# Kernel optimization log

Measured on AMD Instinct MI355X. Metric: run time of the kernel, lower is better.

## Reference

```python
import jax, jax.numpy as jnp
import numpy as np

D = 512      # model dim
H = 8        # heads
HD = D // H  # head dim = 64
NQ = 2048    # n_query
NC = 4096    # n_context
EPS = 1e-5   # LayerNorm eps (torch default)


def setup_inputs() -> dict:
    key = jax.random.key(0)
    ks = jax.random.split(key, 12)
    s = 0.02
    return {
        "query_repr": jax.random.normal(ks[0], (NQ, D), dtype=jnp.float32),
        "context_repr": jax.random.normal(ks[1], (NC, D), dtype=jnp.float32),
        "query_coords": jax.random.uniform(ks[2], (NQ, 2), dtype=jnp.float32) * 10.0,
        "context_coords": jax.random.uniform(ks[3], (NC, 2), dtype=jnp.float32) * 10.0,
        "Wq": jax.random.normal(ks[4], (D, D), dtype=jnp.float32) * s,
        "bq": jnp.zeros((D,), jnp.float32),
        "Wk": jax.random.normal(ks[5], (D, D), dtype=jnp.float32) * s,
        "bk": jnp.zeros((D,), jnp.float32),
        "Wv": jax.random.normal(ks[6], (D, D), dtype=jnp.float32) * s,
        "bv": jnp.zeros((D,), jnp.float32),
        "Wo": jax.random.normal(ks[7], (D, D), dtype=jnp.float32) * s,
        "bo": jnp.zeros((D,), jnp.float32),
        "ln_g": jnp.ones((D,), jnp.float32),
        "ln_b": jnp.zeros((D,), jnp.float32),
        "log_scale": jnp.array(0.0, jnp.float32),          # log_distance_scale
        "bias_per_head": jnp.ones((H,), jnp.float32),      # distance_bias_per_head
    }


def reference(query_repr, context_repr, query_coords, context_coords,
              Wq, bq, Wk, bk, Wv, bv, Wo, bo, ln_g, ln_b,
              log_scale, bias_per_head):
    # pairwise Euclidean distances (NQ, NC)
    diff = query_coords[:, None, :] - context_coords[None, :, :]
    dist = jnp.sqrt(jnp.sum(diff * diff, axis=-1))
    # per-head additive attention bias (H, NQ, NC)
    bias = (-jnp.exp(log_scale) * dist)[None, :, :] * bias_per_head[:, None, None]

    # multi-head attention (batch=1, eval mode so dropout is identity)
    q = (query_repr @ Wq.T + bq).reshape(NQ, H, HD).transpose(1, 0, 2)    # (H, NQ, HD)
    k = (context_repr @ Wk.T + bk).reshape(NC, H, HD).transpose(1, 0, 2)  # (H, NC, HD)
    v = (context_repr @ Wv.T + bv).reshape(NC, H, HD).transpose(1, 0, 2)  # (H, NC, HD)

    scale = 1.0 / jnp.sqrt(jnp.float32(HD))
    scores = jnp.einsum('hqd,hkd->hqk', q, k) * scale + bias              # (H, NQ, NC)
    attn = jax.nn.softmax(scores, axis=-1)
    ctx = jnp.einsum('hqk,hkd->hqd', attn, v)                             # (H, NQ, HD)
    attended = ctx.transpose(1, 0, 2).reshape(NQ, D) @ Wo.T + bo          # (NQ, D)

    # residual + LayerNorm
    x = attended + query_repr
    mu = jnp.mean(x, axis=-1, keepdims=True)
    var = jnp.mean((x - mu) ** 2, axis=-1, keepdims=True)
    return (x - mu) / jnp.sqrt(var + EPS) * ln_g + ln_b
```

## Files before the change

### kernel.cpp

```cpp
#include <hip/hip_runtime.h>

#define D 512
#define H 8
#define HD 64
#define NQ 2048
#define NC 4096
#define SPLIT 8
#define CLEN (NC / SPLIT)
#define NT (CLEN / 32)
#define M0 3.0f
#define KP2 136
#define VP 40

#define TBM 128
#define TBN 64
#define TBK 32
#define TPAD 40

typedef __attribute__((ext_vector_type(8))) short short8;
typedef __attribute__((ext_vector_type(4))) short short4v;
typedef __attribute__((ext_vector_type(4))) float float4v;
typedef __attribute__((ext_vector_type(4))) int int4v;

__device__ inline float bf2f(short s) {
    unsigned int u = ((unsigned int)(unsigned short)s) << 16;
    return __builtin_bit_cast(float, u);
}
__device__ inline short f2bf(float f) {
    unsigned int u = __builtin_bit_cast(unsigned int, f);
    u = (u + 0x7FFF + ((u >> 16) & 1)) >> 16;
    return (short)u;
}
__device__ inline int cvtpk(float a, float b) {
    int w;
    asm("v_cvt_pk_bf16_f32 %0, %1, %2" : "=v"(w) : "v"(a), "v"(b));
    return w;
}

__global__ __launch_bounds__(256) void cast_all(
    const float* __restrict__ s0, const float* __restrict__ s1,
    const float* __restrict__ s2, const float* __restrict__ s3,
    const float* __restrict__ s4, const float* __restrict__ s5,
    short* __restrict__ dst)
{
    int i = blockIdx.x * 256 + threadIdx.x;
    const float* src; int off;
    if      (i < 262144) { src = s0; off = i; }
    else if (i < 786432) { src = s1; off = i - 262144; }
    else if (i < 851968) { src = s2; off = i - 786432; }
    else if (i < 917504) { src = s3; off = i - 851968; }
    else if (i < 983040) { src = s4; off = i - 917504; }
    else                 { src = s5; off = i - 983040; }
    float4v v = ((const float4v*)src)[off];
    short4v o;
    o.x = f2bf(v.x); o.y = f2bf(v.y); o.z = f2bf(v.z); o.w = f2bf(v.w);
    ((short4v*)dst)[i] = o;
}

__global__ __launch_bounds__(256) void gemm_bt_bias(
    const short* __restrict__ X, const short* __restrict__ W,
    const float* __restrict__ bias, short* __restrict__ out, int M)
{
    int wave = threadIdx.x >> 6, lane = threadIdx.x & 63;
    int gt = blockIdx.x * 4 + wave;
    int tm = gt >> 3;
    int tg = gt & 7;
    if (tm >= (M >> 4)) return;
    int l15 = lane & 15, quad = lane >> 4;
    const short* xp = X + (tm * 16 + l15) * D + quad * 8;
    const short* wp = W + (tg * 64 + l15) * D + quad * 8;
    float4v a0 = {0,0,0,0}, a1 = {0,0,0,0}, a2 = {0,0,0,0}, a3 = {0,0,0,0};
#pragma unroll
    for (int k = 0; k < D; k += 32) {
        short8 a  = *(const short8*)(xp + k);
        short8 b0 = *(const short8*)(wp + k);
        short8 b1 = *(const short8*)(wp + 16 * D + k);
        short8 b2 = *(const short8*)(wp + 32 * D + k);
        short8 b3 = *(const short8*)(wp + 48 * D + k);
        a0 = __builtin_amdgcn_mfma_f32_16x16x32_bf16(a, b0, a0, 0, 0, 0);
        a1 = __builtin_amdgcn_mfma_f32_16x16x32_bf16(a, b1, a1, 0, 0, 0);
        a2 = __builtin_amdgcn_mfma_f32_16x16x32_bf16(a, b2, a2, 0, 0, 0);
        a3 = __builtin_amdgcn_mfma_f32_16x16x32_bf16(a, b3, a3, 0, 0, 0);
    }
    int orow = tm * 16 + quad * 4;
    float4v accs[4] = {a0, a1, a2, a3};
#pragma unroll
    for (int j = 0; j < 4; j++) {
        int col = tg * 64 + j * 16 + l15;
        float bv = bias[col];
#pragma unroll
        for (int r = 0; r < 4; r++)
            out[(orow + r) * D + col] = f2bf(accs[j][r] + bv);
    }
}

__global__ __launch_bounds__(256) void gemm_qkv_tiled(
    const short* __restrict__ Xq, const short* __restrict__ Xc,
    const short* __restrict__ Wq, const short* __restrict__ Wk,
    const short* __restrict__ Wv,
    const float* __restrict__ bq, const float* __restrict__ bk,
    const float* __restrict__ bv,
    short* __restrict__ Qout, short* __restrict__ Kout,
    short* __restrict__ VoutT)
{
    __shared__ __align__(16) short Ab[2][TBM * TPAD];
    __shared__ __align__(16) short Bb[2][TBN * TPAD];

    int tid = threadIdx.x;
    int wave = tid >> 6, lane = tid & 63;
    int quad = lane >> 4, l15 = lane & 15;

    int blk = blockIdx.x;
    const short *X, *W;
    const float* bias;
    short* outp;
    int bm, bn, vmode;
    if (blk < 128) {
        X = Xq; W = Wq; bias = bq; outp = Qout; vmode = 0;
        bm = (blk >> 3) * TBM; bn = (blk & 7) * TBN;
    } else if (blk < 384) {
        int b = blk - 128;
        X = Xc; W = Wk; bias = bk; outp = Kout; vmode = 0;
        bm = (b >> 3) * TBM; bn = (b & 7) * TBN;
    } else {
        int b = blk - 384;
        X = Xc; W = Wv; bias = bv; outp = VoutT; vmode = 1;
        bm = (b >> 3) * TBM; bn = (b & 7) * TBN;
    }

    int ar = tid >> 1, ac = (tid & 1) * 16;
    int br = tid >> 2, bc = (tid & 3) * 8;
    const short* ag = X + (size_t)(bm + ar) * D + ac;
    const short* bg = W + (size_t)(bn + br) * D + bc;
    short* aw0 = &Ab[0][ar * TPAD + ac];
    short* aw1 = &Ab[1][ar * TPAD + ac];
    short* bw0 = &Bb[0][br * TPAD + bc];
    short* bw1 = &Bb[1][br * TPAD + bc];

    short8 ra0, ra1, rb;

#define GLOAD(ks) { const short* ap_ = ag + (ks) * TBK;                        \
        ra0 = *(const short8*)(ap_);                                           \
        ra1 = *(const short8*)(ap_ + 8);                                       \
        rb  = *(const short8*)(bg + (ks) * TBK); }
#define GDSW0 { *(short8*)aw0 = ra0; *(short8*)(aw0 + 8) = ra1;                \
                *(short8*)bw0 = rb; }
#define GDSW1 { *(short8*)aw1 = ra0; *(short8*)(aw1 + 8) = ra1;                \
                *(short8*)bw1 = rb; }

    float4v c00 = {0,0,0,0}, c01 = {0,0,0,0}, c02 = {0,0,0,0}, c03 = {0,0,0,0};
    float4v c10 = {0,0,0,0}, c11 = {0,0,0,0}, c12 = {0,0,0,0}, c13 = {0,0,0,0};

#define GCOMP(B)                                                               \
    {                                                                          \
        const short* abase = &Ab[B][(wave * 32 + l15) * TPAD + quad * 8];      \
        const short* bbase = &Bb[B][l15 * TPAD + quad * 8];                    \
        short8 a0 = *(const short8*)(abase);                                   \
        short8 a1 = *(const short8*)(abase + 16 * TPAD);                       \
        short8 b0 = *(const short8*)(bbase);                                   \
        short8 b1 = *(const short8*)(bbase + 16 * TPAD);                       \
        short8 b2 = *(const short8*)(bbase + 32 * TPAD);                       \
        short8 b3 = *(const short8*)(bbase + 48 * TPAD);                       \
        c00 = __builtin_amdgcn_mfma_f32_16x16x32_bf16(a0, b0, c00, 0, 0, 0);   \
        c01 = __builtin_amdgcn_mfma_f32_16x16x32_bf16(a0, b1, c01, 0, 0, 0);   \
        c02 = __builtin_amdgcn_mfma_f32_16x16x32_bf16(a0, b2, c02, 0, 0, 0);   \
        c03 = __builtin_amdgcn_mfma_f32_16x16x32_bf16(a0, b3, c03, 0, 0, 0);   \
        c10 = __builtin_amdgcn_mfma_f32_16x16x32_bf16(a1, b0, c10, 0, 0, 0);   \
        c11 = __builtin_amdgcn_mfma_f32_16x16x32_bf16(a1, b1, c11, 0, 0, 0);   \
        c12 = __builtin_amdgcn_mfma_f32_16x16x32_bf16(a1, b2, c12, 0, 0, 0);   \
        c13 = __builtin_amdgcn_mfma_f32_16x16x32_bf16(a1, b3, c13, 0, 0, 0);   \
    }

    GLOAD(0);
    GDSW0;
    GLOAD(1);
    __syncthreads();

    for (int t = 0; t < 14; t += 2) {
        GDSW1;
        GLOAD(t + 2);
        GCOMP(0);
        __syncthreads();
        GDSW0;
        GLOAD(t + 3);
        GCOMP(1);
        __syncthreads();
    }
    GDSW1;
    GCOMP(0);
    __syncthreads();
    GCOMP(1);

#undef GLOAD
#undef GDSW0
#undef GDSW1
#undef GCOMP

    float4v accs[2][4] = {{c00, c01, c02, c03}, {c10, c11, c12, c13}};
    if (vmode == 0) {
#pragma unroll
        for (int mf = 0; mf < 2; mf++) {
            int orow = bm + wave * 32 + mf * 16 + quad * 4;
#pragma unroll
            for (int nf = 0; nf < 4; nf++) {
                int col = bn + nf * 16 + l15;
                float bb_ = bias[col];
#pragma unroll
                for (int r = 0; r < 4; r++)
                    outp[(size_t)(orow + r) * D + col] = f2bf(accs[mf][nf][r] + bb_);
            }
        }
    } else {
#pragma unroll
        for (int mf = 0; mf < 2; mf++) {
            int orow = bm + wave * 32 + mf * 16 + quad * 4;
            int a = (orow & 31) >> 2;
            int posb = (a < 4) ? (8 * a) : (8 * (a - 4) + 4);
            int cp = (orow & ~31) + posb;
#pragma unroll
            for (int nf = 0; nf < 4; nf++) {
                int col = bn + nf * 16 + l15;
                float bb_ = bias[col];
                short4v o;
#pragma unroll
                for (int r = 0; r < 4; r++) o[r] = f2bf(accs[mf][nf][r] + bb_);
                *(short4v*)(outp + (size_t)col * NC + cp) = o;
            }
        }
    }
}

__global__ __launch_bounds__(256) void gemm_out_tiled(
    const short* __restrict__ X, const short* __restrict__ W,
    const float* __restrict__ bias, const float* __restrict__ resid,
    float* __restrict__ out)
{
    __shared__ __align__(16) short Ab[2][TBM * TPAD];
    __shared__ __align__(16) short Bb[2][TBN * TPAD];

    int tid = threadIdx.x;
    int wave = tid >> 6, lane = tid & 63;
    int quad = lane >> 4, l15 = lane & 15;

    int blk = blockIdx.x;
    int bm = (blk >> 3) * TBM, bn = (blk & 7) * TBN;

    int ar = tid >> 1, ac = (tid & 1) * 16;
    int br = tid >> 2, bc = (tid & 3) * 8;
    const short* ag = X + (size_t)(bm + ar) * D + ac;
    const short* bg = W + (size_t)(bn + br) * D + bc;
    short* aw0 = &Ab[0][ar * TPAD + ac];
    short* aw1 = &Ab[1][ar * TPAD + ac];
    short* bw0 = &Bb[0][br * TPAD + bc];
    short* bw1 = &Bb[1][br * TPAD + bc];

    short8 ra0, ra1, rb;

#define GLOAD(ks) { const short* ap_ = ag + (ks) * TBK;                        \
        ra0 = *(const short8*)(ap_);                                           \
        ra1 = *(const short8*)(ap_ + 8);                                       \
        rb  = *(const short8*)(bg + (ks) * TBK); }
#define GDSW0 { *(short8*)aw0 = ra0; *(short8*)(aw0 + 8) = ra1;                \
                *(short8*)bw0 = rb; }
#define GDSW1 { *(short8*)aw1 = ra0; *(short8*)(aw1 + 8) = ra1;                \
                *(short8*)bw1 = rb; }

    float4v c00 = {0,0,0,0}, c01 = {0,0,0,0}, c02 = {0,0,0,0}, c03 = {0,0,0,0};
    float4v c10 = {0,0,0,0}, c11 = {0,0,0,0}, c12 = {0,0,0,0}, c13 = {0,0,0,0};

#define GCOMP(B)                                                               \
    {                                                                          \
        const short* abase = &Ab[B][(wave * 32 + l15) * TPAD + quad * 8];      \
        const short* bbase = &Bb[B][l15 * TPAD + quad * 8];                    \
        short8 a0 = *(const short8*)(abase);                                   \
        short8 a1 = *(const short8*)(abase + 16 * TPAD);                       \
        short8 b0 = *(const short8*)(bbase);                                   \
        short8 b1 = *(const short8*)(bbase + 16 * TPAD);                       \
        short8 b2 = *(const short8*)(bbase + 32 * TPAD);                       \
        short8 b3 = *(const short8*)(bbase + 48 * TPAD);                       \
        c00 = __builtin_amdgcn_mfma_f32_16x16x32_bf16(a0, b0, c00, 0, 0, 0);   \
        c01 = __builtin_amdgcn_mfma_f32_16x16x32_bf16(a0, b1, c01, 0, 0, 0);   \
        c02 = __builtin_amdgcn_mfma_f32_16x16x32_bf16(a0, b2, c02, 0, 0, 0);   \
        c03 = __builtin_amdgcn_mfma_f32_16x16x32_bf16(a0, b3, c03, 0, 0, 0);   \
        c10 = __builtin_amdgcn_mfma_f32_16x16x32_bf16(a1, b0, c10, 0, 0, 0);   \
        c11 = __builtin_amdgcn_mfma_f32_16x16x32_bf16(a1, b1, c11, 0, 0, 0);   \
        c12 = __builtin_amdgcn_mfma_f32_16x16x32_bf16(a1, b2, c12, 0, 0, 0);   \
        c13 = __builtin_amdgcn_mfma_f32_16x16x32_bf16(a1, b3, c13, 0, 0, 0);   \
    }

    GLOAD(0);
    GDSW0;
    GLOAD(1);
    __syncthreads();

    for (int t = 0; t < 14; t += 2) {
        GDSW1;
        GLOAD(t + 2);
        GCOMP(0);
        __syncthreads();
        GDSW0;
        GLOAD(t + 3);
        GCOMP(1);
        __syncthreads();
    }
    GDSW1;
    GCOMP(0);
    __syncthreads();
    GCOMP(1);

#undef GLOAD
#undef GDSW0
#undef GDSW1
#undef GCOMP

    float4v accs[2][4] = {{c00, c01, c02, c03}, {c10, c11, c12, c13}};
#pragma unroll
    for (int mf = 0; mf < 2; mf++) {
        int orow = bm + wave * 32 + mf * 16 + quad * 4;
#pragma unroll
        for (int nf = 0; nf < 4; nf++) {
            int col = bn + nf * 16 + l15;
            float bb_ = bias[col];
#pragma unroll
            for (int r = 0; r < 4; r++)
                out[(size_t)(orow + r) * D + col] =
                    accs[mf][nf][r] + bb_ + resid[(size_t)(orow + r) * D + col];
        }
    }
}

__global__ __launch_bounds__(256) void gemm_bt_bias_res_f32(
    const short* __restrict__ X, const short* __restrict__ W,
    const float* __restrict__ bias, const float* __restrict__ resid,
    float* __restrict__ out, int M)
{
    int wave = threadIdx.x >> 6, lane = threadIdx.x & 63;
    int gt = blockIdx.x * 4 + wave;
    int tm = gt >> 3;
    int tg = gt & 7;
    if (tm >= (M >> 4)) return;
    int l15 = lane & 15, quad = lane >> 4;
    const short* xp = X + (tm * 16 + l15) * D + quad * 8;
    const short* wp = W + (tg * 64 + l15) * D + quad * 8;
    float4v a0 = {0,0,0,0}, a1 = {0,0,0,0}, a2 = {0,0,0,0}, a3 = {0,0,0,0};
#pragma unroll
    for (int k = 0; k < D; k += 32) {
        short8 a  = *(const short8*)(xp + k);
        short8 b0 = *(const short8*)(wp + k);
        short8 b1 = *(const short8*)(wp + 16 * D + k);
        short8 b2 = *(const short8*)(wp + 32 * D + k);
        short8 b3 = *(const short8*)(wp + 48 * D + k);
        a0 = __builtin_amdgcn_mfma_f32_16x16x32_bf16(a, b0, a0, 0, 0, 0);
        a1 = __builtin_amdgcn_mfma_f32_16x16x32_bf16(a, b1, a1, 0, 0, 0);
        a2 = __builtin_amdgcn_mfma_f32_16x16x32_bf16(a, b2, a2, 0, 0, 0);
        a3 = __builtin_amdgcn_mfma_f32_16x16x32_bf16(a, b3, a3, 0, 0, 0);
    }
    int orow = tm * 16 + quad * 4;
    float4v accs[4] = {a0, a1, a2, a3};
#pragma unroll
    for (int j = 0; j < 4; j++) {
        int col = tg * 64 + j * 16 + l15;
        float bv = bias[col];
#pragma unroll
        for (int r = 0; r < 4; r++) {
            int q = orow + r;
            out[q * D + col] = accs[j][r] + bv + resid[q * D + col];
        }
    }
}

__global__ __launch_bounds__(256) void attn_mfma_split9(
    const short* __restrict__ Q, const short* __restrict__ K,
    const short* __restrict__ Vp,
    const float* __restrict__ qc, const float* __restrict__ cc,
    const float* __restrict__ log_scale, const float* __restrict__ bph,
    short* __restrict__ Opart, float* __restrict__ Lpart)
{
    __shared__ __align__(16) short Klds[2][32 * KP2];
    __shared__ __align__(16) short Vlds[2][128 * VP];
    __shared__ __align__(16) float ccl[512];

    int tid = threadIdx.x;
    int wave = tid >> 6, lane = tid & 63;
    int h0 = blockIdx.y * 2;
    int sp = blockIdx.z;
    int q0 = blockIdx.x * 64 + wave * 16;
    int quad = lane >> 4, l15 = lane & 15;
    int cbase = sp * CLEN;

    const float LOG2E = 1.4426950408889634f;
    const float escale = 0.125f * LOG2E;
    const float M0L = M0 * LOG2E;
    float ebase = __expf(log_scale[0]);
    float bh0 = ebase * bph[h0] * LOG2E;
    float bh1 = ebase * bph[h0 + 1] * LOG2E;

    const short* qp = Q + (q0 + l15) * D + h0 * HD + quad * 8;
    short8 qa0_0 = *(const short8*)(qp);
    short8 qa1_0 = *(const short8*)(qp + 32);
    short8 qa0_1 = *(const short8*)(qp + 64);
    short8 qa1_1 = *(const short8*)(qp + 96);

    float qx = qc[(q0 + l15) * 2];
    float qy = qc[(q0 + l15) * 2 + 1];

    float lacc0 = 0.f, lacc1 = 0.f;
    float4v O00 = {0,0,0,0}, O01 = {0,0,0,0}, O02 = {0,0,0,0}, O03 = {0,0,0,0};
    float4v O10 = {0,0,0,0}, O11 = {0,0,0,0}, O12 = {0,0,0,0}, O13 = {0,0,0,0};

    int kr_ = tid >> 3, kc_ = tid & 7;
    int vr_ = tid >> 2, vc_ = tid & 3;
    const short* kg  = K + (size_t)h0 * HD + kc_ * 8;
    const short* vg0 = Vp + (size_t)(h0 * HD + vr_) * NC + vc_ * 8;
    const short* vg1 = Vp + (size_t)(h0 * HD + 64 + vr_) * NC + vc_ * 8;
    short* kw0a = &Klds[0][kr_ * KP2 + kc_ * 8];
    short* kw1a = &Klds[1][kr_ * KP2 + kc_ * 8];
    short* vw0a = &Vlds[0][vr_ * VP + vc_ * 8];
    short* vw0b = &Vlds[0][(64 + vr_) * VP + vc_ * 8];
    short* vw1a = &Vlds[1][vr_ * VP + vc_ * 8];
    short* vw1b = &Vlds[1][(64 + vr_) * VP + vc_ * 8];

    short8 rka, rkb, rva, rvb;

#define LOADR(c0_)                                                             \
    {                                                                          \
        const short* kp_ = kg + (size_t)((c0_) + kr_) * D;                     \
        rka = *(const short8*)(kp_);                                           \
        rkb = *(const short8*)(kp_ + 64);                                      \
        rva = *(const short8*)(vg0 + (c0_));                                   \
        rvb = *(const short8*)(vg1 + (c0_));                                   \
    }

#define DSW0 { *(short8*)kw0a = rka; *(short8*)(kw0a + 64) = rkb;              \
               *(short8*)vw0a = rva; *(short8*)vw0b = rvb; }
#define DSW1 { *(short8*)kw1a = rka; *(short8*)(kw1a + 64) = rkb;              \
               *(short8*)vw1a = rva; *(short8*)vw1b = rvb; }

    const float2* ccp = (const float2*)ccl;

#define HEAD(hoff, QA0, QA1, BH, LACC, OA, OB, OC, OD)                         \
    {                                                                          \
        short8 k00 = *(const short8*)(kb + l15 * KP2 + (hoff) + quad * 8);     \
        short8 k01 = *(const short8*)(kb + l15 * KP2 + (hoff) + 32 + quad * 8);\
        short8 k10 = *(const short8*)(kb + (16 + l15) * KP2 + (hoff) + quad * 8);\
        short8 k11 = *(const short8*)(kb + (16 + l15) * KP2 + (hoff) + 32 + quad * 8);\
        float4v s0 = {0,0,0,0}, s1 = {0,0,0,0};                                \
        s0 = __builtin_amdgcn_mfma_f32_16x16x32_bf16(k00, QA0, s0, 0, 0, 0);   \
        s0 = __builtin_amdgcn_mfma_f32_16x16x32_bf16(k01, QA1, s0, 0, 0, 0);   \
        s1 = __builtin_amdgcn_mfma_f32_16x16x32_bf16(k10, QA0, s1, 0, 0, 0);   \
        s1 = __builtin_amdgcn_mfma_f32_16x16x32_bf16(k11, QA1, s1, 0, 0, 0);   \
        short8 v0 = *(const short8*)(vb + ((hoff) / 64 * 64 + l15) * VP + quad * 8);       \
        short8 v1 = *(const short8*)(vb + ((hoff) / 64 * 64 + 16 + l15) * VP + quad * 8);  \
        short8 v2 = *(const short8*)(vb + ((hoff) / 64 * 64 + 32 + l15) * VP + quad * 8);  \
        short8 v3 = *(const short8*)(vb + ((hoff) / 64 * 64 + 48 + l15) * VP + quad * 8);  \
        float p00 = exp2f(__fmaf_rn(s0[0], escale, __fmaf_rn(-(BH), dA0, -M0L)));\
        float p01 = exp2f(__fmaf_rn(s0[1], escale, __fmaf_rn(-(BH), dA1, -M0L)));\
        float p02 = exp2f(__fmaf_rn(s0[2], escale, __fmaf_rn(-(BH), dA2, -M0L)));\
        float p03 = exp2f(__fmaf_rn(s0[3], escale, __fmaf_rn(-(BH), dA3, -M0L)));\
        float p10 = exp2f(__fmaf_rn(s1[0], escale, __fmaf_rn(-(BH), dB0, -M0L)));\
        float p11 = exp2f(__fmaf_rn(s1[1], escale, __fmaf_rn(-(BH), dB1, -M0L)));\
        float p12 = exp2f(__fmaf_rn(s1[2], escale, __fmaf_rn(-(BH), dB2, -M0L)));\
        float p13 = exp2f(__fmaf_rn(s1[3], escale, __fmaf_rn(-(BH), dB3, -M0L)));\
        LACC += ((p00 + p01) + (p02 + p03)) + ((p10 + p11) + (p12 + p13));     \
        int4v pw;                                                              \
        pw.x = cvtpk(p00, p01); pw.y = cvtpk(p02, p03);                        \
        pw.z = cvtpk(p10, p11); pw.w = cvtpk(p12, p13);                        \
        short8 pa = __builtin_bit_cast(short8, pw);                            \
        OA = __builtin_amdgcn_mfma_f32_16x16x32_bf16(pa, v0, OA, 0, 0, 0);     \
        OB = __builtin_amdgcn_mfma_f32_16x16x32_bf16(pa, v1, OB, 0, 0, 0);     \
        OC = __builtin_amdgcn_mfma_f32_16x16x32_bf16(pa, v2, OC, 0, 0, 0);     \
        OD = __builtin_amdgcn_mfma_f32_16x16x32_bf16(pa, v3, OD, 0, 0, 0);     \
    }

#define COMPUTE_TILE(B, lo)                                                    \
    {                                                                          \
        const short* kb = &Klds[B][0];                                         \
        const short* vb = &Vlds[B][0];                                         \
        float2 ca0 = ccp[(lo) + 4 * quad + 0], cb0 = ccp[(lo) + 16 + 4 * quad + 0];\
        float2 ca1 = ccp[(lo) + 4 * quad + 1], cb1 = ccp[(lo) + 16 + 4 * quad + 1];\
        float2 ca2 = ccp[(lo) + 4 * quad + 2], cb2 = ccp[(lo) + 16 + 4 * quad + 2];\
        float2 ca3 = ccp[(lo) + 4 * quad + 3], cb3 = ccp[(lo) + 16 + 4 * quad + 3];\
        float dx, dy;                                                          \
        dx = qx - ca0.x; dy = qy - ca0.y;                                      \
        float dA0 = __builtin_amdgcn_sqrtf(__fmaf_rn(dx, dx, dy * dy));        \
        dx = qx - ca1.x; dy = qy - ca1.y;                                      \
        float dA1 = __builtin_amdgcn_sqrtf(__fmaf_rn(dx, dx, dy * dy));        \
        dx = qx - ca2.x; dy = qy - ca2.y;                                      \
        float dA2 = __builtin_amdgcn_sqrtf(__fmaf_rn(dx, dx, dy * dy));        \
        dx = qx - ca3.x; dy = qy - ca3.y;                                      \
        float dA3 = __builtin_amdgcn_sqrtf(__fmaf_rn(dx, dx, dy * dy));        \
        dx = qx - cb0.x; dy = qy - cb0.y;                                      \
        float dB0 = __builtin_amdgcn_sqrtf(__fmaf_rn(dx, dx, dy * dy));        \
        dx = qx - cb1.x; dy = qy - cb1.y;                                      \
        float dB1 = __builtin_amdgcn_sqrtf(__fmaf_rn(dx, dx, dy * dy));        \
        dx = qx - cb2.x; dy = qy - cb2.y;                                      \
        float dB2 = __builtin_amdgcn_sqrtf(__fmaf_rn(dx, dx, dy * dy));        \
        dx = qx - cb3.x; dy = qy - cb3.y;                                      \
        float dB3 = __builtin_amdgcn_sqrtf(__fmaf_rn(dx, dx, dy * dy));        \
        HEAD(0,  qa0_0, qa1_0, bh0, lacc0, O00, O01, O02, O03)                 \
        HEAD(64, qa0_1, qa1_1, bh1, lacc1, O10, O11, O12, O13)                 \
    }

    ((float2*)ccl)[tid] = ((const float2*)cc)[cbase + tid];
    LOADR(cbase);
    DSW0;
    LOADR(cbase + 32);
    __syncthreads();

    for (int t = 0; t < NT - 2; t += 2) {
        int c0 = cbase + t * 32;
        if (t == 8) {
            ((float2*)ccl)[tid] = ((const float2*)cc)[cbase + 256 + tid];
            __syncthreads();
        }
        DSW1;
        LOADR(c0 + 64);
        COMPUTE_TILE(0, (t & 7) * 32);
        __syncthreads();
        DSW0;
        LOADR(c0 + 96);
        COMPUTE_TILE(1, (t & 7) * 32 + 32);
        __syncthreads();
    }
    DSW1;
    COMPUTE_TILE(0, 192);
    __syncthreads();
    COMPUTE_TILE(1, 224);

#undef LOADR
#undef DSW0
#undef DSW1
#undef HEAD
#undef COMPUTE_TILE

    lacc0 += __shfl_xor(lacc0, 16);
    lacc0 += __shfl_xor(lacc0, 32);
    lacc1 += __shfl_xor(lacc1, 16);
    lacc1 += __shfl_xor(lacc1, 32);

    long base0 = (long)(sp * H + h0) * NQ;
    long base1 = base0 + NQ;
    float4v Oarr0[4] = {O00, O01, O02, O03};
    float4v Oarr1[4] = {O10, O11, O12, O13};
#pragma unroll
    for (int t = 0; t < 4; t++) {
#pragma unroll
        for (int r = 0; r < 4; r++) {
            int q = q0 + quad * 4 + r;
            Opart[(base0 + q) * HD + t * 16 + l15] = f2bf(Oarr0[t][r]);
            Opart[(base1 + q) * HD + t * 16 + l15] = f2bf(Oarr1[t][r]);
        }
    }
    if (lane < 16) {
        Lpart[base0 + q0 + lane] = lacc0;
        Lpart[base1 + q0 + lane] = lacc1;
    }
}

__global__ __launch_bounds__(256) void attn_combine(
    const short* __restrict__ Opart, const float* __restrict__ Lpart,
    short* __restrict__ Att)
{
    int id = blockIdx.x * 256 + threadIdx.x;
    int d = id & 63;
    int q = (id >> 6) & (NQ - 1);
    int h = id >> 17;
    float L = 0.f, acc = 0.f;
#pragma unroll
    for (int s = 0; s < SPLIT; s++) {
        long b = (long)(s * H + h) * NQ + q;
        L   += Lpart[b];
        acc += bf2f(Opart[b * HD + d]);
    }
    Att[q * D + h * HD + d] = f2bf(acc / L);
}

__global__ __launch_bounds__(256) void attn_mfma(
    const short* __restrict__ Q, const short* __restrict__ K,
    const short* __restrict__ V,
    const float* __restrict__ qc, const float* __restrict__ cc,
    const float* __restrict__ log_scale, const float* __restrict__ bph,
    short* __restrict__ out)
{
    __shared__ short Vt[HD][48];
    __shared__ short P[4][16][48];
    int wave = threadIdx.x >> 6, lane = threadIdx.x & 63;
    int h = blockIdx.y;
    int q0 = blockIdx.x * 64 + wave * 16;
    int quad = lane >> 4, l15 = lane & 15;
    const float scale = 0.125f;
    float bh = __expf(log_scale[0]) * bph[h];
    const short* qp = Q + (q0 + l15) * D + h * HD + quad * 8;
    short8 qa0 = *(const short8*)(qp);
    short8 qa1 = *(const short8*)(qp + 32);
    float qx[4], qy[4];
#pragma unroll
    for (int r = 0; r < 4; r++) {
        int q = q0 + quad * 4 + r;
        qx[r] = qc[q * 2]; qy[r] = qc[q * 2 + 1];
    }
    float m[4], l[4];
    float4v O[4];
#pragma unroll
    for (int r = 0; r < 4; r++) { m[r] = -1e30f; l[r] = 0.f; }
#pragma unroll
    for (int t = 0; t < 4; t++) O[t] = (float4v){0.f, 0.f, 0.f, 0.f};
    for (int c0 = 0; c0 < NC; c0 += 32) {
        __syncthreads();
        {
            int c = threadIdx.x >> 3;
            int dblk = (threadIdx.x & 7) * 8;
            short8 vv = *(const short8*)(V + (c0 + c) * D + h * HD + dblk);
#pragma unroll
            for (int j = 0; j < 8; j++) Vt[dblk + j][c] = vv[j];
        }
        const short* kp0 = K + (c0 + l15) * D + h * HD + quad * 8;
        const short* kp1 = kp0 + 16 * D;
        short8 kb00 = *(const short8*)(kp0);
        short8 kb01 = *(const short8*)(kp0 + 32);
        short8 kb10 = *(const short8*)(kp1);
        short8 kb11 = *(const short8*)(kp1 + 32);
        float4v s0 = {0,0,0,0}, s1 = {0,0,0,0};
        s0 = __builtin_amdgcn_mfma_f32_16x16x32_bf16(qa0, kb00, s0, 0, 0, 0);
        s0 = __builtin_amdgcn_mfma_f32_16x16x32_bf16(qa1, kb01, s0, 0, 0, 0);
        s1 = __builtin_amdgcn_mfma_f32_16x16x32_bf16(qa0, kb10, s1, 0, 0, 0);
        s1 = __builtin_amdgcn_mfma_f32_16x16x32_bf16(qa1, kb11, s1, 0, 0, 0);
        int cA = c0 + l15, cB = cA + 16;
        float cxA = cc[cA * 2], cyA = cc[cA * 2 + 1];
        float cxB = cc[cB * 2], cyB = cc[cB * 2 + 1];
#pragma unroll
        for (int r = 0; r < 4; r++) {
            float dxA = qx[r] - cxA, dyA = qy[r] - cyA;
            float dxB = qx[r] - cxB, dyB = qy[r] - cyB;
            float v0 = s0[r] * scale - bh * sqrtf(dxA * dxA + dyA * dyA);
            float v1 = s1[r] * scale - bh * sqrtf(dxB * dxB + dyB * dyB);
            float mx = fmaxf(v0, v1);
#pragma unroll
            for (int off = 1; off < 16; off <<= 1) mx = fmaxf(mx, __shfl_xor(mx, off));
            float mnew = fmaxf(m[r], mx);
            float alpha = __expf(m[r] - mnew);
            float p0 = __expf(v0 - mnew);
            float p1 = __expf(v1 - mnew);
            float ps = p0 + p1;
#pragma unroll
            for (int off = 1; off < 16; off <<= 1) ps += __shfl_xor(ps, off);
            l[r] = l[r] * alpha + ps;
            m[r] = mnew;
#pragma unroll
            for (int t = 0; t < 4; t++) O[t][r] *= alpha;
            P[wave][quad * 4 + r][l15]      = f2bf(p0);
            P[wave][quad * 4 + r][16 + l15] = f2bf(p1);
        }
        __syncthreads();
        short8 pa = *(const short8*)(&P[wave][l15][quad * 8]);
#pragma unroll
        for (int t = 0; t < 4; t++) {
            short8 vb = *(const short8*)(&Vt[t * 16 + l15][quad * 8]);
            O[t] = __builtin_amdgcn_mfma_f32_16x16x32_bf16(pa, vb, O[t], 0, 0, 0);
        }
    }
#pragma unroll
    for (int t = 0; t < 4; t++) {
#pragma unroll
        for (int r = 0; r < 4; r++) {
            int q = q0 + quad * 4 + r;
            out[q * D + h * HD + t * 16 + l15] = f2bf(O[t][r] / l[r]);
        }
    }
}

__global__ __launch_bounds__(256) void layernorm_kernel(
    const float* __restrict__ X, const float* __restrict__ g,
    const float* __restrict__ b, float* __restrict__ out)
{
    int wave = threadIdx.x >> 6, lane = threadIdx.x & 63;
    int row = blockIdx.x * 4 + wave;
    const float* xp = X + row * D;
    float v[8];
    float s = 0.f;
#pragma unroll
    for (int i = 0; i < 8; i++) { v[i] = xp[lane + i * 64]; s += v[i]; }
#pragma unroll
    for (int off = 1; off < 64; off <<= 1) s += __shfl_xor(s, off);
    float mu = s * (1.f / D);
    float var = 0.f;
#pragma unroll
    for (int i = 0; i < 8; i++) { float d = v[i] - mu; var += d * d; }
#pragma unroll
    for (int off = 1; off < 64; off <<= 1) var += __shfl_xor(var, off);
    float rstd = rsqrtf(var * (1.f / D) + 1e-5f);
#pragma unroll
    for (int i = 0; i < 8; i++) {
        int c = lane + i * 64;
        out[row * D + c] = (v[i] - mu) * rstd * g[c] + b[c];
    }
}

extern "C" void kernel_launch(void* const* d_in, const int* in_sizes, int n_in,
                              void* d_out, int out_size, void* d_ws, size_t ws_size,
                              hipStream_t stream) {
    const float* query_repr     = (const float*)d_in[0];
    const float* context_repr   = (const float*)d_in[1];
    const float* query_coords   = (const float*)d_in[2];
    const float* context_coords = (const float*)d_in[3];
    const float* Wq = (const float*)d_in[4];
    const float* bq = (const float*)d_in[5];
    const float* Wk = (const float*)d_in[6];
    const float* bk = (const float*)d_in[7];
    const float* Wv = (const float*)d_in[8];
    const float* bv = (const float*)d_in[9];
    const float* Wo = (const float*)d_in[10];
    const float* bo = (const float*)d_in[11];
    const float* ln_g = (const float*)d_in[12];
    const float* ln_b = (const float*)d_in[13];
    const float* log_scale = (const float*)d_in[14];
    const float* bph = (const float*)d_in[15];

    short* ws = (short*)d_ws;
    short* Xq_bf = ws;
    short* Xc_bf = Xq_bf + NQ * D;
    short* Wq_bf = Xc_bf + NC * D;
    short* Wk_bf = Wq_bf + D * D;
    short* Wv_bf = Wk_bf + D * D;
    short* Wo_bf = Wv_bf + D * D;
    short* Qw  = Wo_bf + D * D;
    short* Kw  = Qw + NQ * D;
    short* Vw  = Kw + NC * D;
    short* Att = Vw + NC * D;
    float* Xf  = (float*)(Att + NQ * D);
    short* Opart = (short*)(Xf + NQ * D);
    float* Lpart = (float*)(Opart + (size_t)SPLIT * H * NQ * HD);
    size_t ws_needed_split = ((char*)(Lpart + (size_t)SPLIT * H * NQ)) - (char*)d_ws;

    cast_all<<<dim3(4096), 256, 0, stream>>>(
        query_repr, context_repr, Wq, Wk, Wv, Wo, Xq_bf);

    if (ws_size >= ws_needed_split) {
        gemm_qkv_tiled<<<dim3(640), 256, 0, stream>>>(
            Xq_bf, Xc_bf, Wq_bf, Wk_bf, Wv_bf, bq, bk, bv, Qw, Kw, Vw);
        attn_mfma_split9<<<dim3(NQ / 64, H / 2, SPLIT), 256, 0, stream>>>(
            Qw, Kw, Vw, query_coords, context_coords, log_scale, bph,
            Opart, Lpart);
        attn_combine<<<dim3(H * NQ * HD / 256), 256, 0, stream>>>(
            Opart, Lpart, Att);
        gemm_out_tiled<<<dim3(128), 256, 0, stream>>>(
            Att, Wo_bf, bo, query_repr, Xf);
        layernorm_kernel<<<dim3(NQ / 4), 256, 0, stream>>>(
            Xf, ln_g, ln_b, (float*)d_out);
    } else {
        gemm_bt_bias<<<dim3((NQ / 16) * 8 / 4), 256, 0, stream>>>(
            Xq_bf, Wq_bf, bq, Qw, NQ);
        gemm_bt_bias<<<dim3((NC / 16) * 8 / 4), 256, 0, stream>>>(
            Xc_bf, Wk_bf, bk, Kw, NC);
        gemm_bt_bias<<<dim3((NC / 16) * 8 / 4), 256, 0, stream>>>(
            Xc_bf, Wv_bf, bv, Vw, NC);
        attn_mfma<<<dim3(NQ / 64, H), 256, 0, stream>>>(
            Qw, Kw, Vw, query_coords, context_coords, log_scale, bph, Att);
        gemm_bt_bias_res_f32<<<dim3((NQ / 16) * 8 / 4), 256, 0, stream>>>(
            Att, Wo_bf, bo, query_repr, Xf, NQ);
        layernorm_kernel<<<dim3(NQ / 4), 256, 0, stream>>>(
            Xf, ln_g, ln_b, (float*)d_out);
    }
}
```

Measured before the change: 170.0 us.

## Fuse activation bf16 cast into QKV GEMM and remap attention grid to XCDs

The separate cast of query and context activations is removed. The QKV GEMM now loads fp32 activations and packs them to bf16 on the fly, and a smaller kernel casts only the weights. This avoids writing and rereading the bf16 activation copies and shrinks the cast launch. The attention launch is also flattened to a 1D grid with a swizzled block index (d&7)*128+(d>>3), likely so blocks sharing K/V land on the same XCD and reuse its L2. The cost is that every N-tile block now reads the fp32 activations, twice the bytes, and does the conversion itself.

```diff
diff --git a/kernel.cpp b/kernel.cpp
--- a/kernel.cpp
+++ b/kernel.cpp
@@ -57,6 +57,23 @@
     ((short4v*)dst)[i] = o;
 }
 
+__global__ __launch_bounds__(256) void cast_w(
+    const float* __restrict__ s0, const float* __restrict__ s1,
+    const float* __restrict__ s2, const float* __restrict__ s3,
+    short* __restrict__ dst)
+{
+    int i = blockIdx.x * 256 + threadIdx.x;
+    const float* src; int off;
+    if      (i < 65536)  { src = s0; off = i; }
+    else if (i < 131072) { src = s1; off = i - 65536; }
+    else if (i < 196608) { src = s2; off = i - 131072; }
+    else                 { src = s3; off = i - 196608; }
+    float4v v = ((const float4v*)src)[off];
+    short4v o;
+    o.x = f2bf(v.x); o.y = f2bf(v.y); o.z = f2bf(v.z); o.w = f2bf(v.w);
+    ((short4v*)dst)[i] = o;
+}
+
 __global__ __launch_bounds__(256) void gemm_bt_bias(
     const short* __restrict__ X, const short* __restrict__ W,
     const float* __restrict__ bias, short* __restrict__ out, int M)
@@ -94,8 +111,8 @@
     }
 }
 
-__global__ __launch_bounds__(256) void gemm_qkv_tiled(
-    const short* __restrict__ Xq, const short* __restrict__ Xc,
+__global__ __launch_bounds__(256) void gemm_qkv_tiled_f32(
+    const float* __restrict__ Xqf, const float* __restrict__ Xcf,
     const short* __restrict__ Wq, const short* __restrict__ Wk,
     const short* __restrict__ Wv,
     const float* __restrict__ bq, const float* __restrict__ bk,
@@ -111,26 +128,27 @@
     int quad = lane >> 4, l15 = lane & 15;
 
     int blk = blockIdx.x;
-    const short *X, *W;
+    const float* Xf;
+    const short* W;
     const float* bias;
     short* outp;
     int bm, bn, vmode;
     if (blk < 128) {
-        X = Xq; W = Wq; bias = bq; outp = Qout; vmode = 0;
+        Xf = Xqf; W = Wq; bias = bq; outp = Qout; vmode = 0;
         bm = (blk >> 3) * TBM; bn = (blk & 7) * TBN;
     } else if (blk < 384) {
         int b = blk - 128;
-        X = Xc; W = Wk; bias = bk; outp = Kout; vmode = 0;
+        Xf = Xcf; W = Wk; bias = bk; outp = Kout; vmode = 0;
         bm = (b >> 3) * TBM; bn = (b & 7) * TBN;
     } else {
         int b = blk - 384;
-        X = Xc; W = Wv; bias = bv; outp = VoutT; vmode = 1;
+        Xf = Xcf; W = Wv; bias = bv; outp = VoutT; vmode = 1;
         bm = (b >> 3) * TBM; bn = (b & 7) * TBN;
     }
 
     int ar = tid >> 1, ac = (tid & 1) * 16;
     int br = tid >> 2, bc = (tid & 3) * 8;
-    const short* ag = X + (size_t)(bm + ar) * D + ac;
+    const float* ag = Xf + (size_t)(bm + ar) * D + ac;
     const short* bg = W + (size_t)(bn + br) * D + bc;
     short* aw0 = &Ab[0][ar * TPAD + ac];
     short* aw1 = &Ab[1][ar * TPAD + ac];
@@ -139,9 +157,19 @@
 
     short8 ra0, ra1, rb;
 
-#define GLOAD(ks) { const short* ap_ = ag + (ks) * TBK;                        \
-        ra0 = *(const short8*)(ap_);                                           \
-        ra1 = *(const short8*)(ap_ + 8);                                       \
+#define GLOAD(ks) {                                                            \
+        const float* ap_ = ag + (ks) * TBK;                                    \
+        float4v f0 = *(const float4v*)(ap_);                                   \
+        float4v f1 = *(const float4v*)(ap_ + 4);                               \
+        float4v f2 = *(const float4v*)(ap_ + 8);                               \
+        float4v f3 = *(const float4v*)(ap_ + 12);                              \
+        int4v w0, w1;                                                          \
+        w0.x = cvtpk(f0.x, f0.y); w0.y = cvtpk(f0.z, f0.w);                    \
+        w0.z = cvtpk(f1.x, f1.y); w0.w = cvtpk(f1.z, f1.w);                    \
+        w1.x = cvtpk(f2.x, f2.y); w1.y = cvtpk(f2.z, f2.w);                    \
+        w1.z = cvtpk(f3.x, f3.y); w1.w = cvtpk(f3.z, f3.w);                    \
+        ra0 = __builtin_bit_cast(short8, w0);                                  \
+        ra1 = __builtin_bit_cast(short8, w1);                                  \
         rb  = *(const short8*)(bg + (ks) * TBK); }
 #define GDSW0 { *(short8*)aw0 = ra0; *(short8*)(aw0 + 8) = ra1;                \
                 *(short8*)bw0 = rb; }
@@ -369,7 +397,7 @@
     }
 }
 
-__global__ __launch_bounds__(256) void attn_mfma_split9(
+__global__ __launch_bounds__(256) void attn_mfma_split10(
     const short* __restrict__ Q, const short* __restrict__ K,
     const short* __restrict__ Vp,
     const float* __restrict__ qc, const float* __restrict__ cc,
@@ -382,9 +410,16 @@
 
     int tid = threadIdx.x;
     int wave = tid >> 6, lane = tid & 63;
-    int h0 = blockIdx.y * 2;
-    int sp = blockIdx.z;
-    int q0 = blockIdx.x * 64 + wave * 16;
+
+    int d = blockIdx.x;
+    int s = (d & 7) * 128 + (d >> 3);
+    int bx = s & 31;
+    int by = (s >> 5) & 3;
+    int bz = s >> 7;
+
+    int h0 = by * 2;
+    int sp = bz;
+    int q0 = bx * 64 + wave * 16;
     int quad = lane >> 4, l15 = lane & 15;
     int cbase = sp * CLEN;
 
@@ -732,13 +767,12 @@
     float* Lpart = (float*)(Opart + (size_t)SPLIT * H * NQ * HD);
     size_t ws_needed_split = ((char*)(Lpart + (size_t)SPLIT * H * NQ)) - (char*)d_ws;
 
-    cast_all<<<dim3(4096), 256, 0, stream>>>(
-        query_repr, context_repr, Wq, Wk, Wv, Wo, Xq_bf);
-
     if (ws_size >= ws_needed_split) {
-        gemm_qkv_tiled<<<dim3(640), 256, 0, stream>>>(
-            Xq_bf, Xc_bf, Wq_bf, Wk_bf, Wv_bf, bq, bk, bv, Qw, Kw, Vw);
-        attn_mfma_split9<<<dim3(NQ / 64, H / 2, SPLIT), 256, 0, stream>>>(
+        cast_w<<<dim3(1024), 256, 0, stream>>>(Wq, Wk, Wv, Wo, Wq_bf);
+        gemm_qkv_tiled_f32<<<dim3(640), 256, 0, stream>>>(
+            query_repr, context_repr, Wq_bf, Wk_bf, Wv_bf, bq, bk, bv,
+            Qw, Kw, Vw);
+        attn_mfma_split10<<<dim3(1024), 256, 0, stream>>>(
             Qw, Kw, Vw, query_coords, context_coords, log_scale, bph,
             Opart, Lpart);
         attn_combine<<<dim3(H * NQ * HD / 256), 256, 0, stream>>>(
@@ -748,6 +782,8 @@
         layernorm_kernel<<<dim3(NQ / 4), 256, 0, stream>>>(
             Xf, ln_g, ln_b, (float*)d_out);
     } else {
+        cast_all<<<dim3(4096), 256, 0, stream>>>(
+            query_repr, context_repr, Wq, Wk, Wv, Wo, Xq_bf);
         gemm_bt_bias<<<dim3((NQ / 16) * 8 / 4), 256, 0, stream>>>(
             Xq_bf, Wq_bf, bq, Qw, NQ);
         gemm_bt_bias<<<dim3((NC / 16) * 8 / 4), 256, 0, stream>>>(
```

New measurement: 174.1 us. 2.4% more time.
